# Optimization experiments

Measured on AMD Instinct MI355X. Metric: run time of the kernel, lower is better.

The kernel has to match this reference:

```python
import jax, jax.numpy as jnp
import numpy as np

B, H, FEAT = 16384, 256, 256
GX, GY, SW = 70, 70, 2


def setup_inputs() -> dict:
    key = jax.random.key(0)
    ks = jax.random.split(key, 10)
    stdv = 1.0 / np.sqrt(H)
    feats = jax.random.normal(ks[0], (B, FEAT), dtype=jnp.float32)
    coords = jax.random.randint(ks[1], (B, 2), 0, 64).astype(jnp.float32)
    input_tensor = jnp.concatenate([feats, coords], axis=1)  # [B, FEAT+2]
    hidden = jax.random.normal(ks[2], (B, H), dtype=jnp.float32)
    u = lambda k, shp: jax.random.uniform(k, shp, jnp.float32, -stdv, stdv)
    return {
        "input_tensor": input_tensor,
        "hidden": hidden,
        "w_ih": u(ks[3], (4 * H, FEAT)),
        "b_ih": u(ks[4], (4 * H,)),
        "w_hh": u(ks[5], (4 * H, H)),
        "b_hh": u(ks[6], (4 * H,)),
        "w_out": u(ks[7], (H, 2 * H)),
        "b_out": u(ks[8], (H,)),
        "memory": jax.random.normal(ks[9], (GX, GY, H), dtype=jnp.float32) * 0.1,
    }


def reference(input_tensor, hidden, w_ih, b_ih, w_hh, b_hh, w_out, b_out, memory):
    feature = input_tensor[:, :-2]
    grid = input_tensor[:, -2:].astype(jnp.int32) + SW  # [B,2]

    gi = feature @ w_ih.T + b_ih  # [B,4H]
    gh = hidden @ w_hh.T + b_hh   # [B,4H]
    i_r, i_i, i_n, i_s = jnp.split(gi, 4, axis=1)
    h_r, h_i, h_n, h_s = jnp.split(gh, 4, axis=1)

    resetgate = jax.nn.sigmoid(i_r + h_r)
    updategate = jax.nn.sigmoid(i_i + h_i)
    spatialgate = jax.nn.sigmoid(i_s + h_s)
    newgate = jnp.tanh(i_n + resetgate * h_n)

    # gather (2*SW+1)^2 neighborhood per sample from spatial memory
    gx = jnp.clip(grid[:, 0], 0, GX - 1)
    gy = jnp.clip(grid[:, 1], 0, GY - 1)
    off = jnp.arange(-SW, SW + 1)  # [K]
    xi = jnp.clip(gx[:, None] + off[None, :], 0, GX - 1)  # [B,K]
    yi = jnp.clip(gy[:, None] + off[None, :], 0, GY - 1)  # [B,K]
    K = 2 * SW + 1
    x_flat = jnp.broadcast_to(xi[:, :, None], (xi.shape[0], K, K)).reshape(xi.shape[0], -1)
    y_flat = jnp.broadcast_to(yi[:, None, :], (yi.shape[0], K, K)).reshape(yi.shape[0], -1)
    context = memory[x_flat, y_flat]  # [B, K*K, H]

    # attention (query is detached in original)
    q = jax.lax.stop_gradient(newgate)  # [B,H]
    attn = jnp.einsum('bh,bkh->bk', q, context)  # [B, K*K]
    attn = jnp.where(attn == 0, -jnp.inf, attn)
    w = jax.nn.softmax(attn, axis=1)
    w = jnp.where(jnp.isnan(w), 0.0, w)
    mix = jnp.einsum('bk,bkh->bh', w, context)  # [B,H]
    combined = jnp.concatenate([mix, q], axis=1)  # [B,2H]
    atten_cs = jnp.tanh(combined @ w_out.T + b_out)  # [B,H]

    curr_state = newgate + spatialgate * atten_cs
    output = curr_state + updategate * (hidden - curr_state)
    return output
```

## Files before the change

### kernel.cpp

```cpp
#include <hip/hip_runtime.h>
#include <stdint.h>

#define B_N 16384
#define H_N 256
#define IN_W 258
#define GX_N 70
#define GY_N 70
#define SW_N 2
#define KK_N 25

typedef __bf16 bf16x8 __attribute__((ext_vector_type(8)));
typedef __bf16 bf16x4 __attribute__((ext_vector_type(4)));
typedef __bf16 bf16x2 __attribute__((ext_vector_type(2)));
typedef float f32x4 __attribute__((ext_vector_type(4)));
typedef float f32x2 __attribute__((ext_vector_type(2)));

#define AS1 __attribute__((address_space(1)))
#define AS3 __attribute__((address_space(3)))

static __device__ __forceinline__ void gload16(const void* g, void* l) {
    __builtin_amdgcn_global_load_lds((const AS1 uint32_t*)g, (AS3 uint32_t*)l, 16, 0, 0);
}

#define E_AB   8388608ULL
#define E_WF   8912896ULL
#define E_WOUT 9043968ULL
#define E_COMB 9043968ULL
#define E_UGSG 17432576ULL

__global__ __launch_bounds__(256) void cast_kernel(
    const float* __restrict__ in_t, const float* __restrict__ hid,
    const float* __restrict__ wih, const float* __restrict__ whh,
    const float* __restrict__ wout, __bf16* __restrict__ dst)
{
    size_t g = (size_t)blockIdx.x * blockDim.x + threadIdx.x;
    size_t stride = (size_t)gridDim.x * blockDim.x;
    for (size_t e = g * 4; e < E_WOUT; e += stride * 4) {
        bf16x4 o;
        if (e < E_AB) {
            size_t row = e >> 9;
            size_t c = e & 511;
            if (c < 256) {
                const f32x2* s2 = reinterpret_cast<const f32x2*>(in_t + row * IN_W + c);
                f32x2 a = s2[0], b = s2[1];
                o.x = (__bf16)a.x; o.y = (__bf16)a.y;
                o.z = (__bf16)b.x; o.w = (__bf16)b.y;
            } else {
                f32x4 v = *reinterpret_cast<const f32x4*>(hid + row * 256 + (c - 256));
                o.x = (__bf16)v.x; o.y = (__bf16)v.y;
                o.z = (__bf16)v.z; o.w = (__bf16)v.w;
            }
        } else if (e < E_WF) {
            size_t off = e - E_AB;
            size_t j = off >> 9;
            size_t k = off & 511;
            size_t c = j >> 8;
            size_t col = j & 255;
            size_t base = (c == 0) ? 0 : (c == 1) ? 256 : (c == 2) ? 768 : 512;
            const float* srcm = (k < 256) ? wih : whh;
            f32x4 v = *reinterpret_cast<const f32x4*>(srcm + (base + col) * 256 + (k & 255));
            o.x = (__bf16)v.x; o.y = (__bf16)v.y;
            o.z = (__bf16)v.z; o.w = (__bf16)v.w;
        } else {
            f32x4 v = *reinterpret_cast<const f32x4*>(wout + (e - E_WF));
            o.x = (__bf16)v.x; o.y = (__bf16)v.y;
            o.z = (__bf16)v.z; o.w = (__bf16)v.w;
        }
        *reinterpret_cast<bf16x4*>(dst + e) = o;
    }
}

__global__ __launch_bounds__(256, 2) void gates_gemm(
    const __bf16* __restrict__ AB, const __bf16* __restrict__ wfull,
    const float* __restrict__ b_ih, const float* __restrict__ b_hh,
    __bf16* __restrict__ comb, __bf16* __restrict__ ugsg)
{
    __shared__ __bf16 ldsA[2][4096];
    __shared__ __bf16 ldsB[2][4096];
    const int t = threadIdx.x;
    const int lane = t & 63, w = t >> 6;
    const int lr = lane & 15, seg = lane >> 4;
    const int rb = blockIdx.x * 128;
    const int h0 = blockIdx.y * 32;

    const int rA = t & 127;
    const int sA = t >> 7;
    const __bf16* gAt = AB + (size_t)(rb + rA) * 512 + sA * 8;
    const int bc = rA >> 5, bcol = rA & 31;
    const __bf16* gBt = wfull + (size_t)(bc * 256 + h0 + bcol) * 512 + sA * 8;
    __bf16* lA0 = &ldsA[0][t * 8];
    __bf16* lA1 = &ldsA[1][t * 8];
    __bf16* lB0 = &ldsB[0][t * 8];
    __bf16* lB1 = &ldsB[1][t * 8];

    f32x4 acc[2][6], accni[2][2], accnh[2][2];
#pragma unroll
    for (int rh = 0; rh < 2; rh++) {
#pragma unroll
        for (int cn = 0; cn < 6; cn++) acc[rh][cn] = (f32x4){0.f, 0.f, 0.f, 0.f};
        accni[rh][0] = (f32x4){0.f, 0.f, 0.f, 0.f};
        accni[rh][1] = (f32x4){0.f, 0.f, 0.f, 0.f};
        accnh[rh][0] = (f32x4){0.f, 0.f, 0.f, 0.f};
        accnh[rh][1] = (f32x4){0.f, 0.f, 0.f, 0.f};
    }

    gload16(gAt + 0, lA0);
    gload16(gAt + 16, lA0 + 2048);
    gload16(gBt + 0, lB0);
    gload16(gBt + 16, lB0 + 2048);
    __syncthreads();

#pragma unroll 1
    for (int tt = 0; tt < 16; tt++) {
        const int cur = tt & 1;
        if (tt < 15) {
            const int kn = (tt + 1) * 32;
            __bf16* la = cur ? lA0 : lA1;
            __bf16* lb = cur ? lB0 : lB1;
            gload16(gAt + kn, la);
            gload16(gAt + kn + 16, la + 2048);
            gload16(gBt + kn, lb);
            gload16(gBt + kn + 16, lb + 2048);
        }
        const __bf16* cA = ldsA[cur];
        const __bf16* cB = ldsB[cur];
        bf16x8 af[2];
#pragma unroll
        for (int rh = 0; rh < 2; rh++)
            af[rh] = *reinterpret_cast<const bf16x8*>(cA + seg * 1024 + (w * 32 + rh * 16 + lr) * 8);
#pragma unroll
        for (int cn = 0; cn < 6; cn++) {
            const int c = cn >> 1, hh = cn & 1;
            bf16x8 bb = *reinterpret_cast<const bf16x8*>(cB + seg * 1024 + (c * 32 + hh * 16 + lr) * 8);
#pragma unroll
            for (int rh = 0; rh < 2; rh++)
                acc[rh][(c << 1) + hh] = __builtin_amdgcn_mfma_f32_16x16x32_bf16(af[rh], bb, acc[rh][(c << 1) + hh], 0, 0, 0);
        }
        bf16x8 b6 = *reinterpret_cast<const bf16x8*>(cB + seg * 1024 + (96 + lr) * 8);
        bf16x8 b7 = *reinterpret_cast<const bf16x8*>(cB + seg * 1024 + (112 + lr) * 8);
        if (tt < 8) {
#pragma unroll
            for (int rh = 0; rh < 2; rh++) {
                accni[rh][0] = __builtin_amdgcn_mfma_f32_16x16x32_bf16(af[rh], b6, accni[rh][0], 0, 0, 0);
                accni[rh][1] = __builtin_amdgcn_mfma_f32_16x16x32_bf16(af[rh], b7, accni[rh][1], 0, 0, 0);
            }
        } else {
#pragma unroll
            for (int rh = 0; rh < 2; rh++) {
                accnh[rh][0] = __builtin_amdgcn_mfma_f32_16x16x32_bf16(af[rh], b6, accnh[rh][0], 0, 0, 0);
                accnh[rh][1] = __builtin_amdgcn_mfma_f32_16x16x32_bf16(af[rh], b7, accnh[rh][1], 0, 0, 0);
            }
        }
        __syncthreads();
    }

#pragma unroll
    for (int hh = 0; hh < 2; hh++) {
        const int col = h0 + hh * 16 + lr;
        const float br_ = b_ih[col] + b_hh[col];
        const float bi_ = b_ih[col + 256] + b_hh[col + 256];
        const float bs_ = b_ih[col + 768] + b_hh[col + 768];
        const float bni = b_ih[col + 512];
        const float bnh = b_hh[col + 512];
#pragma unroll
        for (int rh = 0; rh < 2; rh++) {
#pragma unroll
            for (int r = 0; r < 4; r++) {
                const int row = rb + w * 32 + rh * 16 + seg * 4 + r;
                float sr = acc[rh][hh][r] + br_;
                float si = acc[rh][2 + hh][r] + bi_;
                float ss = acc[rh][4 + hh][r] + bs_;
                float vni = accni[rh][hh][r] + bni;
                float vnh = accnh[rh][hh][r] + bnh;
                float rg = 1.f / (1.f + __expf(-sr));
                float ug = 1.f / (1.f + __expf(-si));
                float sg = 1.f / (1.f + __expf(-ss));
                float ng = tanhf(vni + rg * vnh);
                comb[(size_t)row * 512 + 256 + col] = (__bf16)ng;
                bf16x2 us;
                us.x = (__bf16)ug;
                us.y = (__bf16)sg;
                *reinterpret_cast<bf16x2*>(ugsg + ((size_t)row * 256 + col) * 2) = us;
            }
        }
    }
}

__global__ __launch_bounds__(256) void attn_kernel(
    const float* __restrict__ in_t, const float* __restrict__ memory,
    __bf16* __restrict__ comb)
{
    __shared__ __bf16 qlds[4][256];
    __shared__ float sclds[4][32];
    const int w = threadIdx.x >> 6;
    const int lane = threadIdx.x & 63;
    const int b = blockIdx.x * 4 + w;
    const float* row_in = in_t + (size_t)b * IN_W;
    int gx = (int)row_in[256] + SW_N;
    int gy = (int)row_in[257] + SW_N;
    gx = min(max(gx, 0), GX_N - 1);
    gy = min(max(gy, 0), GY_N - 1);

    bf16x4 qb = *reinterpret_cast<const bf16x4*>(comb + (size_t)b * 512 + 256 + lane * 4);
    *reinterpret_cast<bf16x4*>(&qlds[w][lane * 4]) = qb;
    __syncthreads();

    if (lane < 50) {
        const int k = lane >> 1, half = lane & 1;
        const int i = k / 5, j = k - i * 5;
        const int xi = min(max(gx + i - SW_N, 0), GX_N - 1);
        const int yj = min(max(gy + j - SW_N, 0), GY_N - 1);
        const float* vp = memory + ((size_t)xi * GY_N + yj) * H_N + half * 128;
        const __bf16* qp = &qlds[w][half * 128];
        float s = 0.f;
#pragma unroll
        for (int mq = 0; mq < 32; mq++) {
            f32x4 v = *reinterpret_cast<const f32x4*>(vp + mq * 4);
            bf16x4 qq = *reinterpret_cast<const bf16x4*>(qp + mq * 4);
            s += (float)qq.x * v.x + (float)qq.y * v.y + (float)qq.z * v.z + (float)qq.w * v.w;
        }
        s += __shfl_xor(s, 1, 64);
        if (half == 0) sclds[w][k] = s;
    }
    __syncthreads();

    float sc[KK_N];
#pragma unroll
    for (int k = 0; k < KK_N; k++) {
        float a = sclds[w][k];
        sc[k] = (a == 0.f) ? -INFINITY : a;
    }
    float mx = -INFINITY;
#pragma unroll
    for (int k = 0; k < KK_N; k++) mx = fmaxf(mx, sc[k]);
    float d = 0.f;
    if (mx > -INFINITY) {
#pragma unroll
        for (int k = 0; k < KK_N; k++) { sc[k] = __expf(sc[k] - mx); d += sc[k]; }
    } else {
#pragma unroll
        for (int k = 0; k < KK_N; k++) sc[k] = 0.f;
    }
    const float inv = (d != 0.f) ? 1.f / d : 0.f;

    f32x4 o = (f32x4){0.f, 0.f, 0.f, 0.f};
#pragma unroll
    for (int k = 0; k < KK_N; k++) {
        const int i = k / 5, j = k % 5;
        const int xi = min(max(gx + i - SW_N, 0), GX_N - 1);
        const int yj = min(max(gy + j - SW_N, 0), GY_N - 1);
        f32x4 v = *reinterpret_cast<const f32x4*>(memory + ((size_t)xi * GY_N + yj) * H_N + lane * 4);
        const float wk = sc[k] * inv;
        o.x += wk * v.x; o.y += wk * v.y; o.z += wk * v.z; o.w += wk * v.w;
    }
    bf16x4 ob;
    ob.x = (__bf16)o.x; ob.y = (__bf16)o.y; ob.z = (__bf16)o.z; ob.w = (__bf16)o.w;
    *reinterpret_cast<bf16x4*>(comb + (size_t)b * 512 + lane * 4) = ob;
}

__global__ __launch_bounds__(256) void out_gemm(
    const __bf16* __restrict__ comb, const __bf16* __restrict__ woB,
    const float* __restrict__ b_out, const __bf16* __restrict__ ugsg,
    const float* __restrict__ hidden, float* __restrict__ out)
{
    __shared__ __bf16 ldsA[2][4096];
    __shared__ __bf16 ldsB[2][2048];
    const int t = threadIdx.x;
    const int lane = t & 63, w = t >> 6;
    const int lr = lane & 15, seg = lane >> 4;
    const int rb = blockIdx.x * 128;
    const int n0 = blockIdx.y * 64;

    const __bf16* gAt = comb + (size_t)(rb + (t & 127)) * 512 + ((t >> 7) << 3);
    const __bf16* gBt = woB + (size_t)(n0 + (t & 63)) * 512 + ((t >> 6) << 3);
    __bf16* lA0 = &ldsA[0][t * 8];
    __bf16* lA1 = &ldsA[1][t * 8];
    __bf16* lB0 = &ldsB[0][t * 8];
    __bf16* lB1 = &ldsB[1][t * 8];

    f32x4 acc[2][4];
#pragma unroll
    for (int rh = 0; rh < 2; rh++)
#pragma unroll
        for (int ct = 0; ct < 4; ct++) acc[rh][ct] = (f32x4){0.f, 0.f, 0.f, 0.f};

    gload16(gAt + 0, lA0);
    gload16(gAt + 16, lA0 + 2048);
    gload16(gBt + 0, lB0);
    __syncthreads();

#pragma unroll 1
    for (int tt = 0; tt < 16; tt++) {
        const int cur = tt & 1;
        if (tt < 15) {
            const int kn = (tt + 1) * 32;
            __bf16* la = cur ? lA0 : lA1;
            __bf16* lb = cur ? lB0 : lB1;
            gload16(gAt + kn, la);
            gload16(gAt + kn + 16, la + 2048);
            gload16(gBt + kn, lb);
        }
        const __bf16* cA = ldsA[cur];
        const __bf16* cB = ldsB[cur];
        bf16x8 af[2];
#pragma unroll
        for (int rh = 0; rh < 2; rh++)
            af[rh] = *reinterpret_cast<const bf16x8*>(cA + seg * 1024 + (w * 32 + rh * 16 + lr) * 8);
#pragma unroll
        for (int ct = 0; ct < 4; ct++) {
            bf16x8 bb = *reinterpret_cast<const bf16x8*>(cB + seg * 512 + (ct * 16 + lr) * 8);
#pragma unroll
            for (int rh = 0; rh < 2; rh++)
                acc[rh][ct] = __builtin_amdgcn_mfma_f32_16x16x32_bf16(af[rh], bb, acc[rh][ct], 0, 0, 0);
        }
        __syncthreads();
    }

#pragma unroll
    for (int ct = 0; ct < 4; ct++) {
        int col = n0 + ct * 16 + lr;
        float bo = b_out[col];
#pragma unroll
        for (int rh = 0; rh < 2; rh++) {
#pragma unroll
            for (int r = 0; r < 4; r++) {
                int row = rb + w * 32 + rh * 16 + seg * 4 + r;
                size_t idx = (size_t)row * 256 + col;
                float acs = tanhf(acc[rh][ct][r] + bo);
                float ng = (float)comb[(size_t)row * 512 + 256 + col];
                bf16x2 us = *reinterpret_cast<const bf16x2*>(ugsg + idx * 2);
                float ug = (float)us.x, sg = (float)us.y;
                float curr = ng + sg * acs;
                out[idx] = curr + ug * (hidden[idx] - curr);
            }
        }
    }
}

extern "C" void kernel_launch(void* const* d_in, const int* in_sizes, int n_in,
                              void* d_out, int out_size, void* d_ws, size_t ws_size,
                              hipStream_t stream) {
    const float* input_t = (const float*)d_in[0];
    const float* hidden  = (const float*)d_in[1];
    const float* w_ih    = (const float*)d_in[2];
    const float* b_ih    = (const float*)d_in[3];
    const float* w_hh    = (const float*)d_in[4];
    const float* b_hh    = (const float*)d_in[5];
    const float* w_out   = (const float*)d_in[6];
    const float* b_out   = (const float*)d_in[7];
    const float* memory  = (const float*)d_in[8];
    float* out = (float*)d_out;

    __bf16* base  = (__bf16*)d_ws;
    __bf16* AB    = base;
    __bf16* wfull = base + E_AB;
    __bf16* woutB = base + E_WF;
    __bf16* comb  = base + E_COMB;
    __bf16* ugsg  = base + E_UGSG;

    cast_kernel<<<4096, 256, 0, stream>>>(input_t, hidden, w_ih, w_hh, w_out, base);
    gates_gemm<<<dim3(128, 8), 256, 0, stream>>>(AB, wfull, b_ih, b_hh, comb, ugsg);
    attn_kernel<<<4096, 256, 0, stream>>>(input_t, memory, comb);
    out_gemm<<<dim3(128, 4), 256, 0, stream>>>(comb, woutB, b_out, ugsg, hidden, out);
}
```

Before: 233.2 us.

## Keep context vectors in registers and reduce attention scores with DPP wave sums

The attention kernel no longer has 50 lanes each compute a half dot product over 128 elements via LDS. Each lane now loads its 4-element slice of all 25 context vectors once into registers. It reduces the per-lane partial dot products across the wave with a DPP row-shift/broadcast sum plus readlane. The same registered vectors are reused for the weighted mix, which removes the second round of global loads and both __syncthreads. The cost is about 100 extra VGPRs for the context values, which may lower occupancy, plus 25 serial wave reductions.

```diff
diff --git a/kernel.cpp b/kernel.cpp
--- a/kernel.cpp
+++ b/kernel.cpp
@@ -186,12 +186,27 @@
     }
 }
 
+template <int CTRL>
+static __device__ __forceinline__ float dpp_add_step(float x) {
+    int xi = __builtin_bit_cast(int, x);
+    int sh = __builtin_amdgcn_update_dpp(0, xi, CTRL, 0xf, 0xf, true);
+    return x + __builtin_bit_cast(float, sh);
+}
+static __device__ __forceinline__ float wave_sum_readlane(float x) {
+    x = dpp_add_step<0x111>(x);
+    x = dpp_add_step<0x112>(x);
+    x = dpp_add_step<0x114>(x);
+    x = dpp_add_step<0x118>(x);
+    x = dpp_add_step<0x142>(x);
+    x = dpp_add_step<0x143>(x);
+    int s = __builtin_amdgcn_readlane(__builtin_bit_cast(int, x), 63);
+    return __builtin_bit_cast(float, s);
+}
+
 __global__ __launch_bounds__(256) void attn_kernel(
     const float* __restrict__ in_t, const float* __restrict__ memory,
     __bf16* __restrict__ comb)
 {
-    __shared__ __bf16 qlds[4][256];
-    __shared__ float sclds[4][32];
     const int w = threadIdx.x >> 6;
     const int lane = threadIdx.x & 63;
     const int b = blockIdx.x * 4 + w;
@@ -201,35 +216,30 @@
     gx = min(max(gx, 0), GX_N - 1);
     gy = min(max(gy, 0), GY_N - 1);
 
+    int xs[5], ys[5];
+#pragma unroll
+    for (int d = 0; d < 5; d++) {
+        xs[d] = min(max(gx + d - SW_N, 0), GX_N - 1);
+        ys[d] = min(max(gy + d - SW_N, 0), GY_N - 1);
+    }
+
     bf16x4 qb = *reinterpret_cast<const bf16x4*>(comb + (size_t)b * 512 + 256 + lane * 4);
-    *reinterpret_cast<bf16x4*>(&qlds[w][lane * 4]) = qb;
-    __syncthreads();
-
-    if (lane < 50) {
-        const int k = lane >> 1, half = lane & 1;
-        const int i = k / 5, j = k - i * 5;
-        const int xi = min(max(gx + i - SW_N, 0), GX_N - 1);
-        const int yj = min(max(gy + j - SW_N, 0), GY_N - 1);
-        const float* vp = memory + ((size_t)xi * GY_N + yj) * H_N + half * 128;
-        const __bf16* qp = &qlds[w][half * 128];
-        float s = 0.f;
-#pragma unroll
-        for (int mq = 0; mq < 32; mq++) {
-            f32x4 v = *reinterpret_cast<const f32x4*>(vp + mq * 4);
-            bf16x4 qq = *reinterpret_cast<const bf16x4*>(qp + mq * 4);
-            s += (float)qq.x * v.x + (float)qq.y * v.y + (float)qq.z * v.z + (float)qq.w * v.w;
-        }
-        s += __shfl_xor(s, 1, 64);
-        if (half == 0) sclds[w][k] = s;
-    }
-    __syncthreads();
-
+    const float q0 = (float)qb.x, q1 = (float)qb.y, q2 = (float)qb.z, q3 = (float)qb.w;
+
+    f32x4 v[KK_N];
     float sc[KK_N];
 #pragma unroll
     for (int k = 0; k < KK_N; k++) {
-        float a = sclds[w][k];
-        sc[k] = (a == 0.f) ? -INFINITY : a;
-    }
+        const int i = k / 5, j = k % 5;
+        const f32x4* cp = reinterpret_cast<const f32x4*>(
+            memory + ((size_t)xs[i] * GY_N + ys[j]) * H_N);
+        v[k] = cp[lane];
+        float p = q0 * v[k].x + q1 * v[k].y + q2 * v[k].z + q3 * v[k].w;
+        sc[k] = wave_sum_readlane(p);
+    }
+
+#pragma unroll
+    for (int k = 0; k < KK_N; k++) sc[k] = (sc[k] == 0.f) ? -INFINITY : sc[k];
     float mx = -INFINITY;
 #pragma unroll
     for (int k = 0; k < KK_N; k++) mx = fmaxf(mx, sc[k]);
@@ -246,12 +256,8 @@
     f32x4 o = (f32x4){0.f, 0.f, 0.f, 0.f};
 #pragma unroll
     for (int k = 0; k < KK_N; k++) {
-        const int i = k / 5, j = k % 5;
-        const int xi = min(max(gx + i - SW_N, 0), GX_N - 1);
-        const int yj = min(max(gy + j - SW_N, 0), GY_N - 1);
-        f32x4 v = *reinterpret_cast<const f32x4*>(memory + ((size_t)xi * GY_N + yj) * H_N + lane * 4);
         const float wk = sc[k] * inv;
-        o.x += wk * v.x; o.y += wk * v.y; o.z += wk * v.z; o.w += wk * v.w;
+        o.x += wk * v[k].x; o.y += wk * v[k].y; o.z += wk * v[k].z; o.w += wk * v[k].w;
     }
     bf16x4 ob;
     ob.x = (__bf16)o.x; ob.y = (__bf16)o.y; ob.z = (__bf16)o.z; ob.w = (__bf16)o.w;
```

Result: faster. 193.2 us (-17.2%).
